# Kernel optimization log

Hardware: AMD Instinct MI355X
Metric: run time of the kernel (lower is better)

Reference implementation:

```python
import math
import jax, jax.numpy as jnp
import numpy as np

NUM_HEADS = 16
D_MODEL = 1024
D_HEAD = 64
D_SEQ = 2048
NUM_LAYERS = 24
BATCH = 2


def setup_inputs() -> dict:
    key = jax.random.key(0)
    ks = jax.random.split(key, 10)
    s = math.sqrt(0.02)
    residual = jax.random.normal(ks[0], (BATCH, D_SEQ, D_MODEL), dtype=jnp.float32)
    W_Q = jax.random.normal(ks[1], (NUM_HEADS, D_MODEL, D_HEAD), dtype=jnp.float32) * s
    W_K = jax.random.normal(ks[2], (NUM_HEADS, D_MODEL, D_HEAD), dtype=jnp.float32) * s
    W_V = jax.random.normal(ks[3], (NUM_HEADS, D_MODEL, D_HEAD), dtype=jnp.float32) * s
    W_O = jax.random.normal(ks[4], (NUM_HEADS * D_HEAD, D_MODEL), dtype=jnp.float32) * s
    W_O = W_O / math.sqrt(NUM_LAYERS)
    b_Q = jax.random.normal(ks[5], (NUM_HEADS, D_HEAD), dtype=jnp.float32) * s
    b_K = jax.random.normal(ks[6], (NUM_HEADS, D_HEAD), dtype=jnp.float32) * s
    b_V = jax.random.normal(ks[7], (NUM_HEADS, D_HEAD), dtype=jnp.float32) * s
    b_O = jax.random.normal(ks[8], (D_MODEL,), dtype=jnp.float32) * s
    return dict(residual=residual, W_Q=W_Q, W_K=W_K, W_V=W_V, W_O=W_O,
                b_Q=b_Q, b_K=b_K, b_V=b_V, b_O=b_O)


def reference(residual, W_Q, W_K, W_V, W_O, b_Q, b_K, b_V, b_O):
    # residual: [b, s, m]; W_{Q,K,V}: [h, m, d]; b_{Q,K,V}: [h, d]
    Q = jnp.einsum('hmd,bsm->bshd', W_Q, residual) + b_Q
    K = jnp.einsum('hmd,bsm->bshd', W_K, residual) + b_K
    V = jnp.einsum('hmd,bsm->bshd', W_V, residual) + b_V
    # full causal score matrix [b, h, s_q, s_k], masked with -inf above diagonal
    QK = jnp.einsum('bqhd,bkhd->bhqk', Q, K)
    seq = residual.shape[1]
    causal = jnp.triu(jnp.ones((seq, seq), dtype=bool), k=1)  # True above diag
    QK_masked = jnp.where(causal, -jnp.inf, QK)
    soft = jax.nn.softmax(QK_masked / math.sqrt(D_HEAD), axis=-1)
    attn = jnp.einsum('bhqk,bkhd->bqhd', soft, V)  # [b, s, h, d]
    multi_head = attn.reshape(attn.shape[0], attn.shape[1], NUM_HEADS * D_HEAD)
    return jnp.einsum('em,bqe->bqm', W_O, multi_head) + b_O
```

## Files before the change

### kernel.cpp

```cpp
#include <hip/hip_runtime.h>
#include <stdint.h>

typedef unsigned short u16;
typedef unsigned long long u64;
typedef _Float16 f16;
typedef __attribute__((ext_vector_type(8))) _Float16 f16x8;
typedef __attribute__((ext_vector_type(4))) float f32x4;
typedef __attribute__((ext_vector_type(16))) float f32x16;
typedef __attribute__((ext_vector_type(4))) unsigned short u16x4;
typedef __attribute__((ext_vector_type(8))) unsigned short u16x8;

#define NHEADS 16
#define DMODEL 1024
#define DHEAD 64
#define SEQ 2048
#define NBATCH 2
#define MROWS (NBATCH * SEQ)
#define NQKV 3072
#define SCQ 0.18033688011112042f

__device__ __forceinline__ u16 f2h(float x) {
  union { f16 h; u16 u; } v;
  v.h = (f16)x;
  return v.u;
}

__device__ __forceinline__ unsigned pk2u(float x, float y) {
  typedef __fp16 fp16x2 __attribute__((ext_vector_type(2)));
  fp16x2 h = __builtin_amdgcn_cvt_pkrtz(x, y);
  union { fp16x2 h; unsigned u; } v; v.h = h;
  return v.u;
}

__device__ __forceinline__ f16x8 mkfrag(unsigned w0, unsigned w1, unsigned w2, unsigned w3) {
  union { unsigned u[4]; f16x8 f; } t;
  t.u[0] = w0; t.u[1] = w1; t.u[2] = w2; t.u[3] = w3;
  return t.f;
}

__device__ __forceinline__ f16x8 vfrag(const char* row, int sz, int F, int hib8) {
  union { u64 u[2]; f16x8 f; } t;
  t.u[0] = *(const u64*)(row + (((2 * F) ^ sz) << 4) + hib8);
  t.u[1] = *(const u64*)(row + (((2 * F + 1) ^ sz) << 4) + hib8);
  return t.f;
}

__device__ __forceinline__ void gload_lds16(const void* g, void* l) {
  __builtin_amdgcn_global_load_lds(
      (const __attribute__((address_space(1))) void*)g,
      (__attribute__((address_space(3))) void*)l, 16, 0, 0);
}

__global__ __launch_bounds__(256) void prep_kernel(
    const float* __restrict__ X,
    const float* __restrict__ WQ, const float* __restrict__ WK,
    const float* __restrict__ WV, const float* __restrict__ WO,
    u16* __restrict__ Xh, u16* __restrict__ Wqkv, u16* __restrict__ Wo) {
  __shared__ u16 lt[64][72];
  int blk = blockIdx.x;
  if (blk < 2048) {
    int i = blk * 256 + threadIdx.x;
    const f32x4* xv = (const f32x4*)(X + (size_t)i * 8);
    f32x4 a = xv[0], b = xv[1];
    u16x8 o;
    o[0] = f2h(a[0]); o[1] = f2h(a[1]); o[2] = f2h(a[2]); o[3] = f2h(a[3]);
    o[4] = f2h(b[0]); o[5] = f2h(b[1]); o[6] = f2h(b[2]); o[7] = f2h(b[3]);
    *(u16x8*)(Xh + (size_t)i * 8) = o;
  } else if (blk < 2816) {
    int bb = blk - 2048;
    int mt = bb & 15, hh = (bb >> 4) & 15, qkv = bb >> 8;
    const float* W = (qkv == 0) ? WQ : (qkv == 1) ? WK : WV;
    int m_in = threadIdx.x >> 2, dq = threadIdx.x & 3;
    const f32x4* sp4 = (const f32x4*)(W + (size_t)hh * (DMODEL * DHEAD) +
                                      (size_t)(mt * 64 + m_in) * DHEAD + dq * 16);
#pragma unroll
    for (int v4 = 0; v4 < 4; ++v4) {
      f32x4 a = sp4[v4];
#pragma unroll
      for (int j = 0; j < 4; ++j) lt[dq * 16 + v4 * 4 + j][m_in] = f2h(a[j]);
    }
    __syncthreads();
    int d_in = threadIdx.x >> 2, mq = threadIdx.x & 3;
    size_t orow = ((size_t)(qkv * 1024 + hh * 64 + d_in)) * DMODEL + mt * 64 + mq * 16;
    u16x8 o0, o1;
#pragma unroll
    for (int j = 0; j < 8; ++j) {
      o0[j] = lt[d_in][mq * 16 + j];
      o1[j] = lt[d_in][mq * 16 + 8 + j];
    }
    *(u16x8*)(Wqkv + orow) = o0;
    *(u16x8*)(Wqkv + orow + 8) = o1;
  } else {
    int bb = blk - 2816;
    int mt = bb & 15, et = bb >> 4;
    int e_in = threadIdx.x >> 2, mq = threadIdx.x & 3;
    const f32x4* sp4 = (const f32x4*)(WO + (size_t)(et * 64 + e_in) * DMODEL + mt * 64 + mq * 16);
#pragma unroll
    for (int v4 = 0; v4 < 4; ++v4) {
      f32x4 a = sp4[v4];
#pragma unroll
      for (int j = 0; j < 4; ++j) lt[mq * 16 + v4 * 4 + j][e_in] = f2h(a[j]);
    }
    __syncthreads();
    int m_in = threadIdx.x >> 2, eq = threadIdx.x & 3;
    size_t orow = (size_t)(mt * 64 + m_in) * DMODEL + et * 64 + eq * 16;
    u16x8 o0, o1;
#pragma unroll
    for (int j = 0; j < 8; ++j) {
      o0[j] = lt[m_in][eq * 16 + j];
      o1[j] = lt[m_in][eq * 16 + 8 + j];
    }
    *(u16x8*)(Wo + orow) = o0;
    *(u16x8*)(Wo + orow + 8) = o1;
  }
}

__global__ __launch_bounds__(256, 2) void gemm_qkv(
    const u16* __restrict__ A, const u16* __restrict__ Bt,
    const float* __restrict__ bq, const float* __restrict__ bk, const float* __restrict__ bv,
    u16* __restrict__ Qo, u16* __restrict__ Ko, u16* __restrict__ Vto) {
  __shared__ u16 lds[2][8192];
  const int tid = threadIdx.x;
  const int wid = tid >> 6, lane = tid & 63, lr = lane & 15, lg = lane >> 4;
  const int wr = wid >> 1, wc = wid & 1;
  const int brow = blockIdx.y * 128, bcol = blockIdx.x * 128;

  f32x4 acc[4][4];
#pragma unroll
  for (int i = 0; i < 4; ++i)
#pragma unroll
    for (int j = 0; j < 4; ++j) acc[i][j] = (f32x4){0.f, 0.f, 0.f, 0.f};

#define STAGE(buf, kt)                                                               \
  {                                                                                  \
    _Pragma("unroll") for (int i = 0; i < 2; ++i) {                                  \
      int idx = tid + i * 256;                                                       \
      gload_lds16(A + (size_t)(brow + (idx >> 2)) * 1024 + (kt) * 32 + (idx & 3) * 8,\
                  (char*)&lds[buf][0] + (wid * 64 + i * 256) * 16);                  \
    }                                                                                \
    _Pragma("unroll") for (int i = 0; i < 2; ++i) {                                  \
      int idx = tid + i * 256;                                                       \
      gload_lds16(Bt + (size_t)(bcol + (idx >> 2)) * 1024 + (kt) * 32 + (idx & 3) * 8,\
                  (char*)&lds[buf][4096] + (wid * 64 + i * 256) * 16);               \
    }                                                                                \
  }

  STAGE(0, 0);
  __syncthreads();
  int cur = 0;
  for (int kt = 0; kt < 32; ++kt) {
    if (kt + 1 < 32) STAGE(cur ^ 1, kt + 1);
    const u16* Ab = &lds[cur][0];
    const u16* Bb = &lds[cur][4096];
    f16x8 a[4], b[4];
#pragma unroll
    for (int ar = 0; ar < 4; ++ar)
      a[ar] = *(const f16x8*)(Ab + (wr * 64 + ar * 16 + lr) * 32 + lg * 8);
#pragma unroll
    for (int bc = 0; bc < 4; ++bc)
      b[bc] = *(const f16x8*)(Bb + (wc * 64 + bc * 16 + lr) * 32 + lg * 8);
#pragma unroll
    for (int ar = 0; ar < 4; ++ar)
#pragma unroll
      for (int bc = 0; bc < 4; ++bc)
        acc[ar][bc] = __builtin_amdgcn_mfma_f32_16x16x32_f16(a[ar], b[bc], acc[ar][bc], 0, 0, 0);
    __syncthreads();
    cur ^= 1;
  }

#pragma unroll
  for (int ar = 0; ar < 4; ++ar) {
    int row0 = brow + wr * 64 + ar * 16 + lg * 4;
    int bb = row0 >> 11, s0 = row0 & 2047;
#pragma unroll
    for (int bc = 0; bc < 4; ++bc) {
      int n = bcol + wc * 64 + bc * 16 + lr;
      int qkv = n >> 10, hd = n & 1023, h = hd >> 6, d = hd & 63;
      float bias = ((qkv == 0) ? bq : (qkv == 1) ? bk : bv)[hd];
      if (qkv < 2) {
        u16* dst = qkv ? Ko : Qo;
        float sc = qkv ? 1.f : SCQ;
        size_t base = ((size_t)(bb * NHEADS + h) * SEQ + s0) * DHEAD + d;
#pragma unroll
        for (int r = 0; r < 4; ++r)
          dst[base + (size_t)r * DHEAD] = f2h((acc[ar][bc][r] + bias) * sc);
      } else {
        u16x4 o;
        o[0] = f2h(acc[ar][bc][0] + bias);
        o[1] = f2h(acc[ar][bc][1] + bias);
        o[2] = f2h(acc[ar][bc][2] + bias);
        o[3] = f2h(acc[ar][bc][3] + bias);
        *(u16x4*)(Vto + ((size_t)(bb * NHEADS + h) * DHEAD + d) * SEQ + s0) = o;
      }
    }
  }
}

__global__ __launch_bounds__(256, 2) void gemm_out(
    const u16* __restrict__ A, const u16* __restrict__ Bt,
    const float* __restrict__ bo, float* __restrict__ Co) {
  __shared__ u16 lds[2][8192];
  const int tid = threadIdx.x;
  const int wid = tid >> 6, lane = tid & 63, lr = lane & 15, lg = lane >> 4;
  const int wr = wid >> 1, wc = wid & 1;
  const int brow = blockIdx.y * 128, bcol = blockIdx.x * 128;

  f32x4 acc[4][4];
#pragma unroll
  for (int i = 0; i < 4; ++i)
#pragma unroll
    for (int j = 0; j < 4; ++j) acc[i][j] = (f32x4){0.f, 0.f, 0.f, 0.f};

  STAGE(0, 0);
  __syncthreads();
  int cur = 0;
  for (int kt = 0; kt < 32; ++kt) {
    if (kt + 1 < 32) STAGE(cur ^ 1, kt + 1);
    const u16* Ab = &lds[cur][0];
    const u16* Bb = &lds[cur][4096];
    f16x8 a[4], b[4];
#pragma unroll
    for (int ar = 0; ar < 4; ++ar)
      a[ar] = *(const f16x8*)(Ab + (wr * 64 + ar * 16 + lr) * 32 + lg * 8);
#pragma unroll
    for (int bc = 0; bc < 4; ++bc)
      b[bc] = *(const f16x8*)(Bb + (wc * 64 + bc * 16 + lr) * 32 + lg * 8);
#pragma unroll
    for (int ar = 0; ar < 4; ++ar)
#pragma unroll
      for (int bc = 0; bc < 4; ++bc)
        acc[ar][bc] = __builtin_amdgcn_mfma_f32_16x16x32_f16(a[ar], b[bc], acc[ar][bc], 0, 0, 0);
    __syncthreads();
    cur ^= 1;
  }
#undef STAGE

#pragma unroll
  for (int ar = 0; ar < 4; ++ar) {
    int row0 = brow + wr * 64 + ar * 16 + lg * 4;
#pragma unroll
    for (int bc = 0; bc < 4; ++bc) {
      int n = bcol + wc * 64 + bc * 16 + lr;
      float bias = bo[n];
#pragma unroll
      for (int r = 0; r < 4; ++r)
        Co[(size_t)(row0 + r) * DMODEL + n] = acc[ar][bc][r] + bias;
    }
  }
}

__global__ __launch_bounds__(256, 2) void attn_kernel(
    const u16* __restrict__ Q, const u16* __restrict__ K,
    const u16* __restrict__ Vt, u16* __restrict__ MH) {
  __shared__ char sh8[65536];
  const int tid = threadIdx.x, wid = tid >> 6, lane = tid & 63;
  const int l31 = lane & 31, hi = lane >> 5;
  const int pairid = wid >> 1;
  const int qsub = wid & 1;
  const int bid = blockIdx.x;
  const int p = bid >> 5, bh = bid & 31;
  const int h = bh & 15, b = bh >> 4;
  const int tA = 31 - p, tB = p;
  const u16* Qb = Q + (size_t)bh * (SEQ * DHEAD);
  const u16* Kb = K + (size_t)bh * (SEQ * DHEAD);
  const u16* Vb = Vt + (size_t)bh * (DHEAD * SEQ);

  const int sw0 = (l31 ^ (l31 >> 3)) & 7, kz0 = sw0 << 4;
  const int r32 = 32 + l31;
  const int sw1 = (r32 ^ (r32 >> 3)) & 7, kz1 = sw1 << 4;
  const int hib = hi * 16, hib8 = hi * 8;

#pragma unroll
  for (int i = 0; i < 2; ++i) {
    int idx = tid + i * 256, row = idx >> 3;
    int sseg = (idx & 7) ^ ((row ^ (row >> 3)) & 7);
    gload_lds16(Qb + (size_t)(tA * 64 + row) * DHEAD + sseg * 8, sh8 + 32768 + idx * 16);
    gload_lds16(Qb + (size_t)(tB * 64 + row) * DHEAD + sseg * 8, sh8 + 40960 + idx * 16);
    gload_lds16(Kb + (size_t)row * DHEAD + sseg * 8, sh8 + idx * 16);
    gload_lds16(Vb + (size_t)row * SEQ + sseg * 8, sh8 + 16384 + idx * 16);
    gload_lds16(Kb + (size_t)(64 + row) * DHEAD + sseg * 8, sh8 + 8192 + idx * 16);
    gload_lds16(Vb + (size_t)row * SEQ + 64 + sseg * 8, sh8 + 24576 + idx * 16);
  }
  __syncthreads();

  f16x8 qfA0, qfA1, qfA2, qfA3, qfB0, qfB1, qfB2, qfB3;
  {
    int row = (qsub << 5) + l31;
    int swz = ((row ^ (row >> 3)) & 7) << 4;
    const char* qa = sh8 + 32768 + row * 128;
    const char* qb = sh8 + 40960 + row * 128;
    qfA0 = *(const f16x8*)(qa + ((hib + 0)  ^ swz));
    qfA1 = *(const f16x8*)(qa + ((hib + 32) ^ swz));
    qfA2 = *(const f16x8*)(qa + ((hib + 64) ^ swz));
    qfA3 = *(const f16x8*)(qa + ((hib + 96) ^ swz));
    qfB0 = *(const f16x8*)(qb + ((hib + 0)  ^ swz));
    qfB1 = *(const f16x8*)(qb + ((hib + 32) ^ swz));
    qfB2 = *(const f16x8*)(qb + ((hib + 64) ^ swz));
    qfB3 = *(const f16x8*)(qb + ((hib + 96) ^ swz));
  }
  __syncthreads();

#pragma unroll
  for (int seg = 0; seg < 2; ++seg) {
    const int t = seg ? tB : tA;
    const f16x8 q0f = seg ? qfB0 : qfA0;
    const f16x8 q1f = seg ? qfB1 : qfA1;
    const f16x8 q2f = seg ? qfB2 : qfA2;
    const f16x8 q3f = seg ? qfB3 : qfA3;

    if (seg == 1) {
#pragma unroll
      for (int i = 0; i < 2; ++i) {
        int idx = tid + i * 256, row = idx >> 3;
        int sseg = (idx & 7) ^ ((row ^ (row >> 3)) & 7);
        gload_lds16(Kb + (size_t)row * DHEAD + sseg * 8, sh8 + idx * 16);
        gload_lds16(Vb + (size_t)row * SEQ + sseg * 8, sh8 + 16384 + idx * 16);
        if (t >= 1) {
          gload_lds16(Kb + (size_t)(64 + row) * DHEAD + sseg * 8, sh8 + 8192 + idx * 16);
          gload_lds16(Vb + (size_t)row * SEQ + 64 + sseg * 8, sh8 + 24576 + idx * 16);
        }
      }
      __syncthreads();
    }

    f32x16 acc0, acc1;
#pragma unroll
    for (int z = 0; z < 16; ++z) { acc0[z] = 0.f; acc1[z] = 0.f; }
    float m = -1e30f, l = 0.f;
    const int qg = t * 64 + (qsub << 5) + l31;
    const int wall = (t >> 1) + 1;

    for (int si = 0; si < wall; ++si) {
      const int off = (si & 1) ? 32768 : 0;
      const int offn = off ^ 32768;
      const int e = 2 * si + 2;
      if (e <= t) {
#pragma unroll
        for (int i = 0; i < 2; ++i) {
          int idx = tid + i * 256, row = idx >> 3;
          int sseg = (idx & 7) ^ ((row ^ (row >> 3)) & 7);
          gload_lds16(Kb + (size_t)(e * 64 + row) * DHEAD + sseg * 8, sh8 + offn + idx * 16);
          gload_lds16(Vb + (size_t)row * SEQ + e * 64 + sseg * 8, sh8 + offn + 16384 + idx * 16);
          if (e + 1 <= t) {
            gload_lds16(Kb + (size_t)((e + 1) * 64 + row) * DHEAD + sseg * 8,
                        sh8 + offn + 8192 + idx * 16);
            gload_lds16(Vb + (size_t)row * SEQ + (e + 1) * 64 + sseg * 8,
                        sh8 + offn + 24576 + idx * 16);
          }
        }
      }
      const int kt = 2 * si + pairid;
      if (kt <= t) {
        const char* kbuf = sh8 + off + pairid * 8192;
        const char* vbuf = sh8 + off + 16384 + pairid * 8192;

        f32x16 s0, s1;
#pragma unroll
        for (int z = 0; z < 16; ++z) { s0[z] = 0.f; s1[z] = 0.f; }
        {
          const char* kb0 = kbuf + l31 * 128;
          const char* kb1 = kbuf + r32 * 128;
          f16x8 kf;
          __builtin_amdgcn_s_setprio(1);
          kf = *(const f16x8*)(kb0 + ((hib + 0)  ^ kz0)); s0 = __builtin_amdgcn_mfma_f32_32x32x16_f16(kf, q0f, s0, 0, 0, 0);
          kf = *(const f16x8*)(kb0 + ((hib + 32) ^ kz0)); s0 = __builtin_amdgcn_mfma_f32_32x32x16_f16(kf, q1f, s0, 0, 0, 0);
          kf = *(const f16x8*)(kb0 + ((hib + 64) ^ kz0)); s0 = __builtin_amdgcn_mfma_f32_32x32x16_f16(kf, q2f, s0, 0, 0, 0);
          kf = *(const f16x8*)(kb0 + ((hib + 96) ^ kz0)); s0 = __builtin_amdgcn_mfma_f32_32x32x16_f16(kf, q3f, s0, 0, 0, 0);
          kf = *(const f16x8*)(kb1 + ((hib + 0)  ^ kz1)); s1 = __builtin_amdgcn_mfma_f32_32x32x16_f16(kf, q0f, s1, 0, 0, 0);
          kf = *(const f16x8*)(kb1 + ((hib + 32) ^ kz1)); s1 = __builtin_amdgcn_mfma_f32_32x32x16_f16(kf, q1f, s1, 0, 0, 0);
          kf = *(const f16x8*)(kb1 + ((hib + 64) ^ kz1)); s1 = __builtin_amdgcn_mfma_f32_32x32x16_f16(kf, q2f, s1, 0, 0, 0);
          kf = *(const f16x8*)(kb1 + ((hib + 96) ^ kz1)); s1 = __builtin_amdgcn_mfma_f32_32x32x16_f16(kf, q3f, s1, 0, 0, 0);
          __builtin_amdgcn_s_setprio(0);
        }

        if (kt == t) {
#pragma unroll
          for (int rr = 0; rr < 16; ++rr) {
            int k0 = kt * 64 + (rr & 3) + 8 * (rr >> 2) + 4 * hi;
            if (k0 > qg) s0[rr] = -1e30f;
            if (k0 + 32 > qg) s1[rr] = -1e30f;
          }
        }

        float tm = s0[0];
#pragma unroll
        for (int rr = 1; rr < 16; ++rr) tm = fmaxf(tm, s0[rr]);
#pragma unroll
        for (int rr = 0; rr < 16; ++rr) tm = fmaxf(tm, s1[rr]);
        tm = fmaxf(tm, __shfl_xor(tm, 32));

        if (!__all(tm <= m + 8.f)) {
          float m2 = fmaxf(m, tm);
          float al = exp2f(m - m2);
          m = m2;
          l *= al;
#pragma unroll
          for (int rr = 0; rr < 16; ++rr) {
            int qp = (rr & 3) + 8 * (rr >> 2) + 4 * hi;
            float af = __shfl(al, qp);
            acc0[rr] *= af;
            acc1[rr] *= af;
          }
        }

        float rs = 0.f;
#pragma unroll
        for (int rr = 0; rr < 16; ++rr) { s0[rr] = exp2f(s0[rr] - m); rs += s0[rr]; }
#pragma unroll
        for (int rr = 0; rr < 16; ++rr) { s1[rr] = exp2f(s1[rr] - m); rs += s1[rr]; }
        rs += __shfl_xor(rs, 32);
        l += rs;

        f16x8 pa0 = mkfrag(pk2u(s0[0],  s0[1]),  pk2u(s0[2],  s0[3]),
                           pk2u(s0[4],  s0[5]),  pk2u(s0[6],  s0[7]));
        f16x8 pa1 = mkfrag(pk2u(s0[8],  s0[9]),  pk2u(s0[10], s0[11]),
                           pk2u(s0[12], s0[13]), pk2u(s0[14], s0[15]));
        f16x8 pa2 = mkfrag(pk2u(s1[0],  s1[1]),  pk2u(s1[2],  s1[3]),
                           pk2u(s1[4],  s1[5]),  pk2u(s1[6],  s1[7]));
        f16x8 pa3 = mkfrag(pk2u(s1[8],  s1[9]),  pk2u(s1[10], s1[11]),
                           pk2u(s1[12], s1[13]), pk2u(s1[14], s1[15]));

        {
          const char* vr0 = vbuf + l31 * 128;
          const char* vr1 = vbuf + r32 * 128;
          __builtin_amdgcn_s_setprio(1);
          acc0 = __builtin_amdgcn_mfma_f32_32x32x16_f16(pa0, vfrag(vr0, sw0, 0, hib8), acc0, 0, 0, 0);
          acc0 = __builtin_amdgcn_mfma_f32_32x32x16_f16(pa1, vfrag(vr0, sw0, 1, hib8), acc0, 0, 0, 0);
          acc0 = __builtin_amdgcn_mfma_f32_32x32x16_f16(pa2, vfrag(vr0, sw0, 2, hib8), acc0, 0, 0, 0);
          acc0 = __builtin_amdgcn_mfma_f32_32x32x16_f16(pa3, vfrag(vr0, sw0, 3, hib8), acc0, 0, 0, 0);
          acc1 = __builtin_amdgcn_mfma_f32_32x32x16_f16(pa0, vfrag(vr1, sw1, 0, hib8), acc1, 0, 0, 0);
          acc1 = __builtin_amdgcn_mfma_f32_32x32x16_f16(pa1, vfrag(vr1, sw1, 1, hib8), acc1, 0, 0, 0);
          acc1 = __builtin_amdgcn_mfma_f32_32x32x16_f16(pa2, vfrag(vr1, sw1, 2, hib8), acc1, 0, 0, 0);
          acc1 = __builtin_amdgcn_mfma_f32_32x32x16_f16(pa3, vfrag(vr1, sw1, 3, hib8), acc1, 0, 0, 0);
          __builtin_amdgcn_s_setprio(0);
        }
      }
      __syncthreads();
    }

    {
      const int slot = (qsub << 6) | (hi << 5) | l31;
      float* z = (float*)(sh8 + (pairid ? 16384 : 0)) + slot * 18;
      z[0] = m; z[1] = l;
#pragma unroll
      for (int rr = 0; rr < 16; ++rr) z[2 + rr] = pairid ? acc0[rr] : acc1[rr];
      __syncthreads();
      const float* y = (const float*)(sh8 + (pairid ? 0 : 16384)) + slot * 18;
      float mb = y[0], lb = y[1];
      float mM = fmaxf(m, mb);
      float aw = exp2f(m - mM), bw = exp2f(mb - mM);
      float lM = l * aw + lb * bw;
      const int d = pairid ? (32 + l31) : l31;
#pragma unroll
      for (int rr = 0; rr < 16; ++rr) {
        int qp = (rr & 3) + 8 * (rr >> 2) + 4 * hi;
        float aF = __shfl(aw, qp), bF = __shfl(bw, qp), lF = __shfl(lM, qp);
        float own = pairid ? acc1[rr] : acc0[rr];
        float val = (own * aF + y[2 + rr] * bF) / lF;
        int q = t * 64 + (qsub << 5) + qp;
        MH[((size_t)(b * SEQ) + q) * DMODEL + h * DHEAD + d] = f2h(val);
      }
      __syncthreads();
    }
  }
}

extern "C" void kernel_launch(void* const* d_in, const int* in_sizes, int n_in,
                              void* d_out, int out_size, void* d_ws, size_t ws_size,
                              hipStream_t stream) {
  const float* residual = (const float*)d_in[0];
  const float* WQ = (const float*)d_in[1];
  const float* WK = (const float*)d_in[2];
  const float* WV = (const float*)d_in[3];
  const float* WO = (const float*)d_in[4];
  const float* bQ = (const float*)d_in[5];
  const float* bK = (const float*)d_in[6];
  const float* bV = (const float*)d_in[7];
  const float* bO = (const float*)d_in[8];
  float* out = (float*)d_out;

  char* w = (char*)d_ws;
  u16* Xh   = (u16*)(w);
  u16* Wqkv = (u16*)(w + ((size_t)8 << 20));
  u16* Wo   = (u16*)(w + ((size_t)14 << 20));
  u16* Qd   = (u16*)(w + ((size_t)16 << 20));
  u16* Kd   = (u16*)(w + ((size_t)24 << 20));
  u16* Vtd  = (u16*)(w + ((size_t)32 << 20));
  u16* MH   = (u16*)(w + ((size_t)40 << 20));

  prep_kernel<<<3072, 256, 0, stream>>>(residual, WQ, WK, WV, WO, Xh, Wqkv, Wo);

  gemm_qkv<<<dim3(NQKV / 128, MROWS / 128), 256, 0, stream>>>(
      Xh, Wqkv, bQ, bK, bV, Qd, Kd, Vtd);

  attn_kernel<<<512, 256, 0, stream>>>(Qd, Kd, Vtd, MH);

  gemm_out<<<dim3(DMODEL / 128, MROWS / 128), 256, 0, stream>>>(MH, Wo, bO, out);
}
```

Before: 117.3 us.

## Split paired q-tiles into separate blocks, halve LDS, raise attention occupancy

The attention kernel now processes one 64-row query tile per block instead of a paired long+short tile, doubling the grid to 1024 blocks and mapping tiles to blocks in a heavy/light interleaved order. LDS drops from 64KB double-buffered to 32KB single-buffered, with K and V loads staggered between the QK and PV phases, and launch bounds rise to 4 blocks per CU. The aim is more resident waves to hide latency and better load balance, at the cost of losing double-buffer prefetch overlap and adding an extra barrier per iteration.

Result: slower. 222.6 us (+89.9%).

```diff
diff --git a/kernel.cpp b/kernel.cpp
--- a/kernel.cpp
+++ b/kernel.cpp
@@ -249,18 +249,19 @@
   }
 }
 
-__global__ __launch_bounds__(256, 2) void attn_kernel(
+__global__ __launch_bounds__(256, 4) void attn_kernel(
     const u16* __restrict__ Q, const u16* __restrict__ K,
     const u16* __restrict__ Vt, u16* __restrict__ MH) {
-  __shared__ char sh8[65536];
+  __shared__ char sh8[32768];
   const int tid = threadIdx.x, wid = tid >> 6, lane = tid & 63;
   const int l31 = lane & 31, hi = lane >> 5;
   const int pairid = wid >> 1;
   const int qsub = wid & 1;
   const int bid = blockIdx.x;
-  const int p = bid >> 5, bh = bid & 31;
+  const int qidx = bid >> 5, bh = bid & 31;
+  const int t = (qidx < 8) ? (31 - qidx) : (qidx < 16) ? (qidx - 8)
+              : (qidx < 24) ? (39 - qidx) : (qidx - 16);
   const int h = bh & 15, b = bh >> 4;
-  const int tA = 31 - p, tB = p;
   const u16* Qb = Q + (size_t)bh * (SEQ * DHEAD);
   const u16* Kb = K + (size_t)bh * (SEQ * DHEAD);
   const u16* Vb = Vt + (size_t)bh * (DHEAD * SEQ);
@@ -274,193 +275,183 @@
   for (int i = 0; i < 2; ++i) {
     int idx = tid + i * 256, row = idx >> 3;
     int sseg = (idx & 7) ^ ((row ^ (row >> 3)) & 7);
-    gload_lds16(Qb + (size_t)(tA * 64 + row) * DHEAD + sseg * 8, sh8 + 32768 + idx * 16);
-    gload_lds16(Qb + (size_t)(tB * 64 + row) * DHEAD + sseg * 8, sh8 + 40960 + idx * 16);
+    gload_lds16(Qb + (size_t)(t * 64 + row) * DHEAD + sseg * 8, sh8 + 16384 + idx * 16);
     gload_lds16(Kb + (size_t)row * DHEAD + sseg * 8, sh8 + idx * 16);
-    gload_lds16(Vb + (size_t)row * SEQ + sseg * 8, sh8 + 16384 + idx * 16);
-    gload_lds16(Kb + (size_t)(64 + row) * DHEAD + sseg * 8, sh8 + 8192 + idx * 16);
-    gload_lds16(Vb + (size_t)row * SEQ + 64 + sseg * 8, sh8 + 24576 + idx * 16);
+    if (t >= 1)
+      gload_lds16(Kb + (size_t)(64 + row) * DHEAD + sseg * 8, sh8 + 8192 + idx * 16);
   }
   __syncthreads();
 
-  f16x8 qfA0, qfA1, qfA2, qfA3, qfB0, qfB1, qfB2, qfB3;
+  f16x8 qf0, qf1, qf2, qf3;
   {
     int row = (qsub << 5) + l31;
     int swz = ((row ^ (row >> 3)) & 7) << 4;
-    const char* qa = sh8 + 32768 + row * 128;
-    const char* qb = sh8 + 40960 + row * 128;
-    qfA0 = *(const f16x8*)(qa + ((hib + 0)  ^ swz));
-    qfA1 = *(const f16x8*)(qa + ((hib + 32) ^ swz));
-    qfA2 = *(const f16x8*)(qa + ((hib + 64) ^ swz));
-    qfA3 = *(const f16x8*)(qa + ((hib + 96) ^ swz));
-    qfB0 = *(const f16x8*)(qb + ((hib + 0)  ^ swz));
-    qfB1 = *(const f16x8*)(qb + ((hib + 32) ^ swz));
-    qfB2 = *(const f16x8*)(qb + ((hib + 64) ^ swz));
-    qfB3 = *(const f16x8*)(qb + ((hib + 96) ^ swz));
+    const char* qb = sh8 + 16384 + row * 128;
+    qf0 = *(const f16x8*)(qb + ((hib + 0)  ^ swz));
+    qf1 = *(const f16x8*)(qb + ((hib + 32) ^ swz));
+    qf2 = *(const f16x8*)(qb + ((hib + 64) ^ swz));
+    qf3 = *(const f16x8*)(qb + ((hib + 96) ^ swz));
   }
   __syncthreads();
 
 #pragma unroll
-  for (int seg = 0; seg < 2; ++seg) {
-    const int t = seg ? tB : tA;
-    const f16x8 q0f = seg ? qfB0 : qfA0;
-    const f16x8 q1f = seg ? qfB1 : qfA1;
-    const f16x8 q2f = seg ? qfB2 : qfA2;
-    const f16x8 q3f = seg ? qfB3 : qfA3;
-
-    if (seg == 1) {
+  for (int i = 0; i < 2; ++i) {
+    int idx = tid + i * 256, row = idx >> 3;
+    int sseg = (idx & 7) ^ ((row ^ (row >> 3)) & 7);
+    gload_lds16(Vb + (size_t)row * SEQ + sseg * 8, sh8 + 16384 + idx * 16);
+    if (t >= 1)
+      gload_lds16(Vb + (size_t)row * SEQ + 64 + sseg * 8, sh8 + 24576 + idx * 16);
+  }
+
+  f32x16 acc0, acc1;
+#pragma unroll
+  for (int z = 0; z < 16; ++z) { acc0[z] = 0.f; acc1[z] = 0.f; }
+  float m = -1e30f, l = 0.f;
+  const int qg = t * 64 + (qsub << 5) + l31;
+  const int wall = (t >> 1) + 1;
+
+  for (int si = 0; si < wall; ++si) {
+    const int kt = 2 * si + pairid;
+    const bool act = (kt <= t);
+    f16x8 pa0, pa1, pa2, pa3;
+
+    if (act) {
+      const char* kbuf = sh8 + pairid * 8192;
+
+      f32x16 s0, s1;
+#pragma unroll
+      for (int z = 0; z < 16; ++z) { s0[z] = 0.f; s1[z] = 0.f; }
+      {
+        const char* kb0 = kbuf + l31 * 128;
+        const char* kb1 = kbuf + r32 * 128;
+        f16x8 kf;
+        __builtin_amdgcn_s_setprio(1);
+        kf = *(const f16x8*)(kb0 + ((hib + 0)  ^ kz0)); s0 = __builtin_amdgcn_mfma_f32_32x32x16_f16(kf, qf0, s0, 0, 0, 0);
+        kf = *(const f16x8*)(kb0 + ((hib + 32) ^ kz0)); s0 = __builtin_amdgcn_mfma_f32_32x32x16_f16(kf, qf1, s0, 0, 0, 0);
+        kf = *(const f16x8*)(kb0 + ((hib + 64) ^ kz0)); s0 = __builtin_amdgcn_mfma_f32_32x32x16_f16(kf, qf2, s0, 0, 0, 0);
+        kf = *(const f16x8*)(kb0 + ((hib + 96) ^ kz0)); s0 = __builtin_amdgcn_mfma_f32_32x32x16_f16(kf, qf3, s0, 0, 0, 0);
+        kf = *(const f16x8*)(kb1 + ((hib + 0)  ^ kz1)); s1 = __builtin_amdgcn_mfma_f32_32x32x16_f16(kf, qf0, s1, 0, 0, 0);
+        kf = *(const f16x8*)(kb1 + ((hib + 32) ^ kz1)); s1 = __builtin_amdgcn_mfma_f32_32x32x16_f16(kf, qf1, s1, 0, 0, 0);
+        kf = *(const f16x8*)(kb1 + ((hib + 64) ^ kz1)); s1 = __builtin_amdgcn_mfma_f32_32x32x16_f16(kf, qf2, s1, 0, 0, 0);
+        kf = *(const f16x8*)(kb1 + ((hib + 96) ^ kz1)); s1 = __builtin_amdgcn_mfma_f32_32x32x16_f16(kf, qf3, s1, 0, 0, 0);
+        __builtin_amdgcn_s_setprio(0);
+      }
+
+      if (kt == t) {
+#pragma unroll
+        for (int rr = 0; rr < 16; ++rr) {
+          int k0 = kt * 64 + (rr & 3) + 8 * (rr >> 2) + 4 * hi;
+          if (k0 > qg) s0[rr] = -1e30f;
+          if (k0 + 32 > qg) s1[rr] = -1e30f;
+        }
+      }
+
+      float tm = s0[0];
+#pragma unroll
+      for (int rr = 1; rr < 16; ++rr) tm = fmaxf(tm, s0[rr]);
+#pragma unroll
+      for (int rr = 0; rr < 16; ++rr) tm = fmaxf(tm, s1[rr]);
+      tm = fmaxf(tm, __shfl_xor(tm, 32));
+
+      if (!__all(tm <= m + 8.f)) {
+        float m2 = fmaxf(m, tm);
+        float al = exp2f(m - m2);
+        m = m2;
+        l *= al;
+#pragma unroll
+        for (int rr = 0; rr < 16; ++rr) {
+          int qp = (rr & 3) + 8 * (rr >> 2) + 4 * hi;
+          float af = __shfl(al, qp);
+          acc0[rr] *= af;
+          acc1[rr] *= af;
+        }
+      }
+
+      float rs = 0.f;
+#pragma unroll
+      for (int rr = 0; rr < 16; ++rr) { s0[rr] = exp2f(s0[rr] - m); rs += s0[rr]; }
+#pragma unroll
+      for (int rr = 0; rr < 16; ++rr) { s1[rr] = exp2f(s1[rr] - m); rs += s1[rr]; }
+      rs += __shfl_xor(rs, 32);
+      l += rs;
+
+      pa0 = mkfrag(pk2u(s0[0],  s0[1]),  pk2u(s0[2],  s0[3]),
+                   pk2u(s0[4],  s0[5]),  pk2u(s0[6],  s0[7]));
+      pa1 = mkfrag(pk2u(s0[8],  s0[9]),  pk2u(s0[10], s0[11]),
+                   pk2u(s0[12], s0[13]), pk2u(s0[14], s0[15]));
+      pa2 = mkfrag(pk2u(s1[0],  s1[1]),  pk2u(s1[2],  s1[3]),
+                   pk2u(s1[4],  s1[5]),  pk2u(s1[6],  s1[7]));
+      pa3 = mkfrag(pk2u(s1[8],  s1[9]),  pk2u(s1[10], s1[11]),
+                   pk2u(s1[12], s1[13]), pk2u(s1[14], s1[15]));
+    }
+
+    __syncthreads();
+
+    const int e = 2 * si + 2;
+    if (e <= t) {
 #pragma unroll
       for (int i = 0; i < 2; ++i) {
         int idx = tid + i * 256, row = idx >> 3;
         int sseg = (idx & 7) ^ ((row ^ (row >> 3)) & 7);
-        gload_lds16(Kb + (size_t)row * DHEAD + sseg * 8, sh8 + idx * 16);
-        gload_lds16(Vb + (size_t)row * SEQ + sseg * 8, sh8 + 16384 + idx * 16);
-        if (t >= 1) {
-          gload_lds16(Kb + (size_t)(64 + row) * DHEAD + sseg * 8, sh8 + 8192 + idx * 16);
-          gload_lds16(Vb + (size_t)row * SEQ + 64 + sseg * 8, sh8 + 24576 + idx * 16);
-        }
-      }
-      __syncthreads();
-    }
-
-    f32x16 acc0, acc1;
-#pragma unroll
-    for (int z = 0; z < 16; ++z) { acc0[z] = 0.f; acc1[z] = 0.f; }
-    float m = -1e30f, l = 0.f;
-    const int qg = t * 64 + (qsub << 5) + l31;
-    const int wall = (t >> 1) + 1;
-
-    for (int si = 0; si < wall; ++si) {
-      const int off = (si & 1) ? 32768 : 0;
-      const int offn = off ^ 32768;
-      const int e = 2 * si + 2;
-      if (e <= t) {
-#pragma unroll
-        for (int i = 0; i < 2; ++i) {
-          int idx = tid + i * 256, row = idx >> 3;
-          int sseg = (idx & 7) ^ ((row ^ (row >> 3)) & 7);
-          gload_lds16(Kb + (size_t)(e * 64 + row) * DHEAD + sseg * 8, sh8 + offn + idx * 16);
-          gload_lds16(Vb + (size_t)row * SEQ + e * 64 + sseg * 8, sh8 + offn + 16384 + idx * 16);
-          if (e + 1 <= t) {
-            gload_lds16(Kb + (size_t)((e + 1) * 64 + row) * DHEAD + sseg * 8,
-                        sh8 + offn + 8192 + idx * 16);
-            gload_lds16(Vb + (size_t)row * SEQ + (e + 1) * 64 + sseg * 8,
-                        sh8 + offn + 24576 + idx * 16);
-          }
-        }
-      }
-      const int kt = 2 * si + pairid;
-      if (kt <= t) {
-        const char* kbuf = sh8 + off + pairid * 8192;
-        const char* vbuf = sh8 + off + 16384 + pairid * 8192;
-
-        f32x16 s0, s1;
-#pragma unroll
-        for (int z = 0; z < 16; ++z) { s0[z] = 0.f; s1[z] = 0.f; }
-        {
-          const char* kb0 = kbuf + l31 * 128;
-          const char* kb1 = kbuf + r32 * 128;
-          f16x8 kf;
-          __builtin_amdgcn_s_setprio(1);
-          kf = *(const f16x8*)(kb0 + ((hib + 0)  ^ kz0)); s0 = __builtin_amdgcn_mfma_f32_32x32x16_f16(kf, q0f, s0, 0, 0, 0);
-          kf = *(const f16x8*)(kb0 + ((hib + 32) ^ kz0)); s0 = __builtin_amdgcn_mfma_f32_32x32x16_f16(kf, q1f, s0, 0, 0, 0);
-          kf = *(const f16x8*)(kb0 + ((hib + 64) ^ kz0)); s0 = __builtin_amdgcn_mfma_f32_32x32x16_f16(kf, q2f, s0, 0, 0, 0);
-          kf = *(const f16x8*)(kb0 + ((hib + 96) ^ kz0)); s0 = __builtin_amdgcn_mfma_f32_32x32x16_f16(kf, q3f, s0, 0, 0, 0);
-          kf = *(const f16x8*)(kb1 + ((hib + 0)  ^ kz1)); s1 = __builtin_amdgcn_mfma_f32_32x32x16_f16(kf, q0f, s1, 0, 0, 0);
-          kf = *(const f16x8*)(kb1 + ((hib + 32) ^ kz1)); s1 = __builtin_amdgcn_mfma_f32_32x32x16_f16(kf, q1f, s1, 0, 0, 0);
-          kf = *(const f16x8*)(kb1 + ((hib + 64) ^ kz1)); s1 = __builtin_amdgcn_mfma_f32_32x32x16_f16(kf, q2f, s1, 0, 0, 0);
-          kf = *(const f16x8*)(kb1 + ((hib + 96) ^ kz1)); s1 = __builtin_amdgcn_mfma_f32_32x32x16_f16(kf, q3f, s1, 0, 0, 0);
-          __builtin_amdgcn_s_setprio(0);
-        }
-
-        if (kt == t) {
-#pragma unroll
-          for (int rr = 0; rr < 16; ++rr) {
-            int k0 = kt * 64 + (rr & 3) + 8 * (rr >> 2) + 4 * hi;
-            if (k0 > qg) s0[rr] = -1e30f;
-            if (k0 + 32 > qg) s1[rr] = -1e30f;
-          }
-        }
-
-        float tm = s0[0];
-#pragma unroll
-        for (int rr = 1; rr < 16; ++rr) tm = fmaxf(tm, s0[rr]);
-#pragma unroll
-        for (int rr = 0; rr < 16; ++rr) tm = fmaxf(tm, s1[rr]);
-        tm = fmaxf(tm, __shfl_xor(tm, 32));
-
-        if (!__all(tm <= m + 8.f)) {
-          float m2 = fmaxf(m, tm);
-          float al = exp2f(m - m2);
-          m = m2;
-          l *= al;
-#pragma unroll
-          for (int rr = 0; rr < 16; ++rr) {
-            int qp = (rr & 3) + 8 * (rr >> 2) + 4 * hi;
-            float af = __shfl(al, qp);
-            acc0[rr] *= af;
-            acc1[rr] *= af;
-          }
-        }
-
-        float rs = 0.f;
-#pragma unroll
-        for (int rr = 0; rr < 16; ++rr) { s0[rr] = exp2f(s0[rr] - m); rs += s0[rr]; }
-#pragma unroll
-        for (int rr = 0; rr < 16; ++rr) { s1[rr] = exp2f(s1[rr] - m); rs += s1[rr]; }
-        rs += __shfl_xor(rs, 32);
-        l += rs;
-
-        f16x8 pa0 = mkfrag(pk2u(s0[0],  s0[1]),  pk2u(s0[2],  s0[3]),
-                           pk2u(s0[4],  s0[5]),  pk2u(s0[6],  s0[7]));
-        f16x8 pa1 = mkfrag(pk2u(s0[8],  s0[9]),  pk2u(s0[10], s0[11]),
-                           pk2u(s0[12], s0[13]), pk2u(s0[14], s0[15]));
-        f16x8 pa2 = mkfrag(pk2u(s1[0],  s1[1]),  pk2u(s1[2],  s1[3]),
-                           pk2u(s1[4],  s1[5]),  pk2u(s1[6],  s1[7]));
-        f16x8 pa3 = mkfrag(pk2u(s1[8],  s1[9]),  pk2u(s1[10], s1[11]),
-                           pk2u(s1[12], s1[13]), pk2u(s1[14], s1[15]));
-
-        {
-          const char* vr0 = vbuf + l31 * 128;
-          const char* vr1 = vbuf + r32 * 128;
-          __builtin_amdgcn_s_setprio(1);
-          acc0 = __builtin_amdgcn_mfma_f32_32x32x16_f16(pa0, vfrag(vr0, sw0, 0, hib8), acc0, 0, 0, 0);
-          acc0 = __builtin_amdgcn_mfma_f32_32x32x16_f16(pa1, vfrag(vr0, sw0, 1, hib8), acc0, 0, 0, 0);
-          acc0 = __builtin_amdgcn_mfma_f32_32x32x16_f16(pa2, vfrag(vr0, sw0, 2, hib8), acc0, 0, 0, 0);
-          acc0 = __builtin_amdgcn_mfma_f32_32x32x16_f16(pa3, vfrag(vr0, sw0, 3, hib8), acc0, 0, 0, 0);
-          acc1 = __builtin_amdgcn_mfma_f32_32x32x16_f16(pa0, vfrag(vr1, sw1, 0, hib8), acc1, 0, 0, 0);
-          acc1 = __builtin_amdgcn_mfma_f32_32x32x16_f16(pa1, vfrag(vr1, sw1, 1, hib8), acc1, 0, 0, 0);
-          acc1 = __builtin_amdgcn_mfma_f32_32x32x16_f16(pa2, vfrag(vr1, sw1, 2, hib8), acc1, 0, 0, 0);
-          acc1 = __builtin_amdgcn_mfma_f32_32x32x16_f16(pa3, vfrag(vr1, sw1, 3, hib8), acc1, 0, 0, 0);
-          __builtin_amdgcn_s_setprio(0);
-        }
-      }
-      __syncthreads();
-    }
-
-    {
-      const int slot = (qsub << 6) | (hi << 5) | l31;
-      float* z = (float*)(sh8 + (pairid ? 16384 : 0)) + slot * 18;
-      z[0] = m; z[1] = l;
-#pragma unroll
-      for (int rr = 0; rr < 16; ++rr) z[2 + rr] = pairid ? acc0[rr] : acc1[rr];
-      __syncthreads();
-      const float* y = (const float*)(sh8 + (pairid ? 0 : 16384)) + slot * 18;
-      float mb = y[0], lb = y[1];
-      float mM = fmaxf(m, mb);
-      float aw = exp2f(m - mM), bw = exp2f(mb - mM);
-      float lM = l * aw + lb * bw;
-      const int d = pairid ? (32 + l31) : l31;
-#pragma unroll
-      for (int rr = 0; rr < 16; ++rr) {
-        int qp = (rr & 3) + 8 * (rr >> 2) + 4 * hi;
-        float aF = __shfl(aw, qp), bF = __shfl(bw, qp), lF = __shfl(lM, qp);
-        float own = pairid ? acc1[rr] : acc0[rr];
-        float val = (own * aF + y[2 + rr] * bF) / lF;
-        int q = t * 64 + (qsub << 5) + qp;
-        MH[((size_t)(b * SEQ) + q) * DMODEL + h * DHEAD + d] = f2h(val);
-      }
-      __syncthreads();
+        gload_lds16(Kb + (size_t)(e * 64 + row) * DHEAD + sseg * 8, sh8 + idx * 16);
+        if (e + 1 <= t)
+          gload_lds16(Kb + (size_t)((e + 1) * 64 + row) * DHEAD + sseg * 8,
+                      sh8 + 8192 + idx * 16);
+      }
+    }
+
+    if (act) {
+      const char* vbuf = sh8 + 16384 + pairid * 8192;
+      const char* vr0 = vbuf + l31 * 128;
+      const char* vr1 = vbuf + r32 * 128;
+      __builtin_amdgcn_s_setprio(1);
+      acc0 = __builtin_amdgcn_mfma_f32_32x32x16_f16(pa0, vfrag(vr0, sw0, 0, hib8), acc0, 0, 0, 0);
+      acc0 = __builtin_amdgcn_mfma_f32_32x32x16_f16(pa1, vfrag(vr0, sw0, 1, hib8), acc0, 0, 0, 0);
+      acc0 = __builtin_amdgcn_mfma_f32_32x32x16_f16(pa2, vfrag(vr0, sw0, 2, hib8), acc0, 0, 0, 0);
+      acc0 = __builtin_amdgcn_mfma_f32_32x32x16_f16(pa3, vfrag(vr0, sw0, 3, hib8), acc0, 0, 0, 0);
+      acc1 = __builtin_amdgcn_mfma_f32_32x32x16_f16(pa0, vfrag(vr1, sw1, 0, hib8), acc1, 0, 0, 0);
+      acc1 = __builtin_amdgcn_mfma_f32_32x32x16_f16(pa1, vfrag(vr1, sw1, 1, hib8), acc1, 0, 0, 0);
+      acc1 = __builtin_amdgcn_mfma_f32_32x32x16_f16(pa2, vfrag(vr1, sw1, 2, hib8), acc1, 0, 0, 0);
+      acc1 = __builtin_amdgcn_mfma_f32_32x32x16_f16(pa3, vfrag(vr1, sw1, 3, hib8), acc1, 0, 0, 0);
+      __builtin_amdgcn_s_setprio(0);
+    }
+
+    __syncthreads();
+
+    if (e <= t) {
+#pragma unroll
+      for (int i = 0; i < 2; ++i) {
+        int idx = tid + i * 256, row = idx >> 3;
+        int sseg = (idx & 7) ^ ((row ^ (row >> 3)) & 7);
+        gload_lds16(Vb + (size_t)row * SEQ + e * 64 + sseg * 8, sh8 + 16384 + idx * 16);
+        if (e + 1 <= t)
+          gload_lds16(Vb + (size_t)row * SEQ + (e + 1) * 64 + sseg * 8,
+                      sh8 + 24576 + idx * 16);
+      }
+    }
+  }
+
+  {
+    const int slot = (qsub << 6) | (hi << 5) | l31;
+    float* z = (float*)(sh8 + (pairid ? 16384 : 0)) + slot * 18;
+    z[0] = m; z[1] = l;
+#pragma unroll
+    for (int rr = 0; rr < 16; ++rr) z[2 + rr] = pairid ? acc0[rr] : acc1[rr];
+    __syncthreads();
+    const float* y = (const float*)(sh8 + (pairid ? 0 : 16384)) + slot * 18;
+    float mb = y[0], lb = y[1];
+    float mM = fmaxf(m, mb);
+    float aw = exp2f(m - mM), bw = exp2f(mb - mM);
+    float lM = l * aw + lb * bw;
+    const int d = pairid ? (32 + l31) : l31;
+#pragma unroll
+    for (int rr = 0; rr < 16; ++rr) {
+      int qp = (rr & 3) + 8 * (rr >> 2) + 4 * hi;
+      float aF = __shfl(aw, qp), bF = __shfl(bw, qp), lF = __shfl(lM, qp);
+      float own = pairid ? acc1[rr] : acc0[rr];
+      float val = (own * aF + y[2 + rr] * bF) / lF;
+      int q = t * 64 + (qsub << 5) + qp;
+      MH[((size_t)(b * SEQ) + q) * DMODEL + h * DHEAD + d] = f2h(val);
     }
   }
 }
@@ -493,7 +484,7 @@
   gemm_qkv<<<dim3(NQKV / 128, MROWS / 128), 256, 0, stream>>>(
       Xh, Wqkv, bQ, bK, bV, Qd, Kd, Vtd);
 
-  attn_kernel<<<512, 256, 0, stream>>>(Qd, Kd, Vtd, MH);
+  attn_kernel<<<1024, 256, 0, stream>>>(Qd, Kd, Vtd, MH);
 
   gemm_out<<<dim3(DMODEL / 128, MROWS / 128), 256, 0, stream>>>(MH, Wo, bO, out);
 }
```
